# Kernel tuning notes

Measured on AMD Instinct MI355X. Metric: run time of the kernel, lower is better.

## Reference

```python
import jax, jax.numpy as jnp
import numpy as np

NUM_ITERATIONS = 10
ALPHA = 0.1


def setup_inputs() -> dict:
    key = jax.random.key(0)
    k1, k2, k3, k4 = jax.random.split(key, 4)
    N, E, F_IN, H = 100000, 3200000, 512, 64
    x = jax.random.normal(k1, (N, F_IN), dtype=jnp.float32)
    edge_index = jax.random.randint(k2, (2, E), 0, N, dtype=jnp.int32)
    edge_weight = jnp.ones((E,), dtype=jnp.float32)
    # glorot-ish scaled dense weights
    W0 = jax.random.normal(k3, (F_IN, H), dtype=jnp.float32) * (2.0 / (F_IN + H)) ** 0.5
    b0 = jnp.zeros((H,), dtype=jnp.float32)
    W1 = jax.random.normal(k4, (H, H), dtype=jnp.float32) * (2.0 / (H + H)) ** 0.5
    b1 = jnp.zeros((H,), dtype=jnp.float32)
    return {"x": x, "edge_index": edge_index, "edge_weight": edge_weight,
            "W0": W0, "b0": b0, "W1": W1, "b1": b1}


def _gcn_norm_edge(edge_index, edge_weight, num_nodes):
    # renorm: add self-loops with weight 1, then symmetric D^-1/2 A D^-1/2
    row, col = edge_index[0], edge_index[1]
    loop = jnp.arange(num_nodes, dtype=edge_index.dtype)
    row = jnp.concatenate([row, loop])
    col = jnp.concatenate([col, loop])
    w = jnp.concatenate([edge_weight, jnp.ones((num_nodes,), edge_weight.dtype)])
    deg = jax.ops.segment_sum(w, row, num_segments=num_nodes)
    dinv = jnp.where(deg > 0, jax.lax.rsqrt(jnp.where(deg > 0, deg, 1.0)), 0.0)
    w_norm = dinv[row] * w * dinv[col]
    return row, col, w_norm


def reference(x, edge_index, edge_weight, W0, b0, W1, b1):
    N = x.shape[0]
    # MLP: hidden layers relu-activated, last layer unactivated
    h = jax.nn.relu(x @ W0 + b0)
    h = h @ W1 + b1  # [N, H]

    row, col, w_norm = _gcn_norm_edge(edge_index, edge_weight, N)

    def step(z, _):
        # sparse propagation: gather at source, weight, scatter-add at dest
        msg = z[row] * w_norm[:, None]                      # [E+N, H]
        agg = jax.ops.segment_sum(msg, col, num_segments=N)  # [N, H]
        return (1.0 - ALPHA) * agg + ALPHA * h, None

    z, _ = jax.lax.scan(step, h, None, length=NUM_ITERATIONS)
    return z
```

## Files before the change

kernel.cpp:

```cpp
#include <hip/hip_runtime.h>


#define PAGE 16128
#define BPP 64

typedef __attribute__((ext_vector_type(8))) short bf16x8;
typedef __attribute__((ext_vector_type(4))) float f32x4;

__device__ __forceinline__ float bf_lo(unsigned z) { return __uint_as_float(z << 16); }
__device__ __forceinline__ float bf_hi(unsigned z) { return __uint_as_float(z & 0xffff0000u); }
__device__ __forceinline__ unsigned bf_rne(float x) {
    unsigned u = __float_as_uint(x);
    return (u + 0x7fffu + ((u >> 16) & 1u)) >> 16;
}
__device__ __forceinline__ unsigned bf_pack(float x, float y) { return bf_rne(x) | (bf_rne(y) << 16); }

__global__ __launch_bounds__(256) void k_deg(const int* __restrict__ row, const float* __restrict__ ew,
                                             float* __restrict__ slab, int E, int chunk) {
    __shared__ float hf[PAGE];
    int p = blockIdx.x / BPP, b = blockIdx.x - p * BPP;
    int lo = p * PAGE;
    for (int i = threadIdx.x; i < PAGE; i += 256) hf[i] = 0.f;
    __syncthreads();
    int e0 = b * chunk, e1 = min(e0 + chunk, E);
    int evec = e0 + ((e1 - e0) & ~3);
    for (int e = e0 + (int)threadIdx.x * 4; e + 4 <= evec; e += 1024) {
        int4 r4 = *(const int4*)(row + e);
        float4 w4 = *(const float4*)(ew + e);
        unsigned a = (unsigned)(r4.x - lo), bq = (unsigned)(r4.y - lo);
        unsigned c = (unsigned)(r4.z - lo), dq = (unsigned)(r4.w - lo);
        if (a < PAGE) atomicAdd(&hf[a], w4.x);
        if (bq < PAGE) atomicAdd(&hf[bq], w4.y);
        if (c < PAGE) atomicAdd(&hf[c], w4.z);
        if (dq < PAGE) atomicAdd(&hf[dq], w4.w);
    }
    for (int e = evec + (int)threadIdx.x; e < e1; e += 256) {
        unsigned a = (unsigned)(row[e] - lo);
        if (a < PAGE) atomicAdd(&hf[a], ew[e]);
    }
    __syncthreads();
    float* out = slab + (size_t)blockIdx.x * PAGE;
    for (int i = threadIdx.x; i < PAGE; i += 256) out[i] = hf[i];
}

__global__ __launch_bounds__(256) void k_fold_deg(const float* __restrict__ slab, float* __restrict__ dinv, int N) {
    int i = blockIdx.x * 256 + threadIdx.x;
    if (i >= N) return;
    int p = i / PAGE, ld = i - p * PAGE;
    const float* base = slab + (size_t)(p * BPP) * PAGE + ld;
    float d = 1.0f;
#pragma unroll
    for (int b = 0; b < BPP; ++b) d += base[(size_t)b * PAGE];
    dinv[i] = d > 0.f ? rsqrtf(d) : 0.f;
}

__global__ __launch_bounds__(256) void k_cnt(const int* __restrict__ col, unsigned short* __restrict__ slab,
                                             int E, int chunk) {
    __shared__ int hi[PAGE];
    int p = blockIdx.x / BPP, b = blockIdx.x - p * BPP;
    int lo = p * PAGE;
    for (int i = threadIdx.x; i < PAGE; i += 256) hi[i] = 0;
    __syncthreads();
    int e0 = b * chunk, e1 = min(e0 + chunk, E);
    int evec = e0 + ((e1 - e0) & ~3);
    for (int e = e0 + (int)threadIdx.x * 4; e + 4 <= evec; e += 1024) {
        int4 c4 = *(const int4*)(col + e);
        unsigned a = (unsigned)(c4.x - lo), bq = (unsigned)(c4.y - lo);
        unsigned c = (unsigned)(c4.z - lo), dq = (unsigned)(c4.w - lo);
        if (a < PAGE) atomicAdd(&hi[a], 1);
        if (bq < PAGE) atomicAdd(&hi[bq], 1);
        if (c < PAGE) atomicAdd(&hi[c], 1);
        if (dq < PAGE) atomicAdd(&hi[dq], 1);
    }
    for (int e = evec + (int)threadIdx.x; e < e1; e += 256) {
        unsigned a = (unsigned)(col[e] - lo);
        if (a < PAGE) atomicAdd(&hi[a], 1);
    }
    __syncthreads();
    unsigned short* out = slab + (size_t)blockIdx.x * PAGE;
    for (int i = threadIdx.x; i < PAGE; i += 256) out[i] = (unsigned short)hi[i];
}

__global__ __launch_bounds__(256) void k_fold_cnt(unsigned short* __restrict__ slab, int* __restrict__ cnt, int N) {
    int i = blockIdx.x * 256 + threadIdx.x;
    if (i >= N) return;
    int p = i / PAGE, ld = i - p * PAGE;
    unsigned short* base = slab + (size_t)(p * BPP) * PAGE + ld;
    int run = 0;
#pragma unroll
    for (int b = 0; b < BPP; ++b) {
        size_t off = (size_t)b * PAGE;
        int v = base[off];
        base[off] = (unsigned short)run;
        run += v;
    }
    cnt[i] = run;
}

__global__ __launch_bounds__(256) void k_scanA(const int* __restrict__ cnt, int* __restrict__ csum, int N) {
    __shared__ int s[256];
    int t = threadIdx.x, base = blockIdx.x * 1024;
    int p = 0;
#pragma unroll
    for (int j = 0; j < 4; ++j) { int idx = base + t + 256 * j; if (idx < N) p += cnt[idx]; }
    s[t] = p; __syncthreads();
    for (int off = 128; off > 0; off >>= 1) { if (t < off) s[t] += s[t + off]; __syncthreads(); }
    if (t == 0) csum[blockIdx.x] = s[0];
}

__global__ __launch_bounds__(256) void k_scanB(int* __restrict__ csum, int NC) {
    __shared__ int s[256];
    int t = threadIdx.x;
    int v = (t < NC) ? csum[t] : 0;
    s[t] = v; __syncthreads();
    for (int off = 1; off < 256; off <<= 1) {
        int x = (t >= off) ? s[t - off] : 0;
        __syncthreads();
        s[t] += x; __syncthreads();
    }
    if (t < NC) csum[t] = s[t] - v;
}

__global__ __launch_bounds__(256) void k_scanC(const int* __restrict__ cnt, const int* __restrict__ csum,
                                               int* __restrict__ rowp, int N) {
    __shared__ int s[256];
    int t = threadIdx.x, base = blockIdx.x * 1024 + t * 4;
    int c0 = (base + 0 < N) ? cnt[base + 0] : 0;
    int c1 = (base + 1 < N) ? cnt[base + 1] : 0;
    int c2 = (base + 2 < N) ? cnt[base + 2] : 0;
    int c3 = (base + 3 < N) ? cnt[base + 3] : 0;
    int ts = c0 + c1 + c2 + c3;
    s[t] = ts; __syncthreads();
    for (int off = 1; off < 256; off <<= 1) {
        int x = (t >= off) ? s[t - off] : 0;
        __syncthreads();
        s[t] += x; __syncthreads();
    }
    int o = csum[blockIdx.x] + s[t] - ts;
    if (base + 0 < N) rowp[base + 0] = o;
    if (base + 1 < N) rowp[base + 1] = o + c0;
    if (base + 2 < N) rowp[base + 2] = o + c0 + c1;
    if (base + 3 < N) rowp[base + 3] = o + c0 + c1 + c2;
}

__global__ __launch_bounds__(256) void k_scat(const int* __restrict__ row, const int* __restrict__ col,
                                              const float* __restrict__ ew, const float* __restrict__ dinv,
                                              const int* __restrict__ rowp, const unsigned short* __restrict__ slab,
                                              unsigned* __restrict__ srcw, int E, int chunk) {
    __shared__ int cur[PAGE];
    int p = blockIdx.x / BPP, b = blockIdx.x - p * BPP;
    int lo = p * PAGE;
    for (int i = threadIdx.x; i < PAGE; i += 256) cur[i] = 0;
    __syncthreads();
    const unsigned short* soff = slab + (size_t)blockIdx.x * PAGE;
    int e0 = b * chunk, e1 = min(e0 + chunk, E);
    int evec = e0 + ((e1 - e0) & ~3);
    for (int e = e0 + (int)threadIdx.x * 4; e + 4 <= evec; e += 1024) {
        int4 c4 = *(const int4*)(col + e);
        unsigned a = (unsigned)(c4.x - lo), bq = (unsigned)(c4.y - lo);
        unsigned cc = (unsigned)(c4.z - lo), dq = (unsigned)(c4.w - lo);
        if ((a < PAGE) | (bq < PAGE) | (cc < PAGE) | (dq < PAGE)) {
            int4 r4 = *(const int4*)(row + e);
            float4 w4 = *(const float4*)(ew + e);
            if (a < PAGE) {
                int pos = rowp[c4.x] + soff[a] + atomicAdd(&cur[a], 1);
                srcw[pos] = ((unsigned)r4.x << 15) | (bf_rne(dinv[r4.x] * w4.x) & 0x7fffu);
            }
            if (bq < PAGE) {
                int pos = rowp[c4.y] + soff[bq] + atomicAdd(&cur[bq], 1);
                srcw[pos] = ((unsigned)r4.y << 15) | (bf_rne(dinv[r4.y] * w4.y) & 0x7fffu);
            }
            if (cc < PAGE) {
                int pos = rowp[c4.z] + soff[cc] + atomicAdd(&cur[cc], 1);
                srcw[pos] = ((unsigned)r4.z << 15) | (bf_rne(dinv[r4.z] * w4.z) & 0x7fffu);
            }
            if (dq < PAGE) {
                int pos = rowp[c4.w] + soff[dq] + atomicAdd(&cur[dq], 1);
                srcw[pos] = ((unsigned)r4.w << 15) | (bf_rne(dinv[r4.w] * w4.w) & 0x7fffu);
            }
        }
    }
    for (int e = evec + (int)threadIdx.x; e < e1; e += 256) {
        int c = col[e];
        unsigned a = (unsigned)(c - lo);
        if (a < PAGE) {
            int r = row[e];
            int pos = rowp[c] + soff[a] + atomicAdd(&cur[a], 1);
            srcw[pos] = ((unsigned)r << 15) | (bf_rne(dinv[r] * ew[e]) & 0x7fffu);
        }
    }
}

__global__ __launch_bounds__(256) void k_wcvt(const float* __restrict__ W,
                                              unsigned short* __restrict__ Th, unsigned short* __restrict__ Tl,
                                              int K, int total) {
    int i = blockIdx.x * 256 + threadIdx.x;
    if (i >= total) return;
    int k = i >> 6, n = i & 63;
    float v = W[i];
    unsigned hi = bf_rne(v);
    float hv = __uint_as_float(hi << 16);
    unsigned lo = bf_rne(v - hv);
    Th[(size_t)n * K + k] = (unsigned short)hi;
    Tl[(size_t)n * K + k] = (unsigned short)lo;
}

__global__ __launch_bounds__(256) void k_mlp(const float* __restrict__ x,
                                             const unsigned short* __restrict__ w0th, const unsigned short* __restrict__ w0tl,
                                             const unsigned short* __restrict__ w1th, const unsigned short* __restrict__ w1tl,
                                             const float* __restrict__ b0, const float* __restrict__ b1,
                                             unsigned* __restrict__ hb, int N) {
    __shared__ __align__(16) unsigned short h1h[64 * 72];
    __shared__ __align__(16) unsigned short h1l[64 * 72];
    int tid = threadIdx.x;
    int w = tid >> 6, lane = tid & 63;
    int g = lane >> 4, r16 = lane & 15;
    int rbase = blockIdx.x * 64;
    int arow = rbase + w * 16 + r16;
    bool rowok = arow < N;
    const float* xp = x + (size_t)arow * 512 + g * 8;

    f32x4 acc[4];
#pragma unroll
    for (int t = 0; t < 4; ++t) acc[t] = (f32x4){0.f, 0.f, 0.f, 0.f};

    for (int ks = 0; ks < 16; ++ks) {
        int k0 = ks * 32;
        float4 v0 = make_float4(0.f, 0.f, 0.f, 0.f), v1 = v0;
        if (rowok) {
            v0 = *(const float4*)(xp + k0);
            v1 = *(const float4*)(xp + k0 + 4);
        }
        float xv[8] = {v0.x, v0.y, v0.z, v0.w, v1.x, v1.y, v1.z, v1.w};
        bf16x8 xh, xl;
#pragma unroll
        for (int e = 0; e < 8; ++e) {
            float xe = xv[e];
            unsigned hi = bf_rne(xe);
            float hv = __uint_as_float(hi << 16);
            unsigned lo = bf_rne(xe - hv);
            xh[e] = (short)hi;
            xl[e] = (short)lo;
        }
#pragma unroll
        for (int t = 0; t < 4; ++t) {
            size_t wo = (size_t)(t * 16 + r16) * 512 + k0 + g * 8;
            bf16x8 wh = *(const bf16x8*)(w0th + wo);
            bf16x8 wl = *(const bf16x8*)(w0tl + wo);
            acc[t] = __builtin_amdgcn_mfma_f32_16x16x32_bf16(xh, wh, acc[t], 0, 0, 0);
            acc[t] = __builtin_amdgcn_mfma_f32_16x16x32_bf16(xl, wh, acc[t], 0, 0, 0);
            acc[t] = __builtin_amdgcn_mfma_f32_16x16x32_bf16(xh, wl, acc[t], 0, 0, 0);
        }
    }
#pragma unroll
    for (int t = 0; t < 4; ++t) {
        int c = t * 16 + r16;
        float bb = b0[c];
#pragma unroll
        for (int r = 0; r < 4; ++r) {
            float v = fmaxf(acc[t][r] + bb, 0.f);
            unsigned hi = bf_rne(v);
            float hv = __uint_as_float(hi << 16);
            unsigned lo = bf_rne(v - hv);
            int rr = w * 16 + g * 4 + r;
            h1h[rr * 72 + c] = (unsigned short)hi;
            h1l[rr * 72 + c] = (unsigned short)lo;
        }
    }
    __syncthreads();
    f32x4 acc2[4];
#pragma unroll
    for (int t = 0; t < 4; ++t) acc2[t] = (f32x4){0.f, 0.f, 0.f, 0.f};
#pragma unroll
    for (int ks = 0; ks < 2; ++ks) {
        int k0 = ks * 32;
        const unsigned short* ap = h1h + (w * 16 + r16) * 72 + k0 + g * 8;
        bf16x8 ah = *(const bf16x8*)ap;
        bf16x8 al = *(const bf16x8*)(ap + 64 * 72);
        al = *(const bf16x8*)(h1l + (w * 16 + r16) * 72 + k0 + g * 8);
#pragma unroll
        for (int t = 0; t < 4; ++t) {
            size_t wo = (size_t)(t * 16 + r16) * 64 + k0 + g * 8;
            bf16x8 wh = *(const bf16x8*)(w1th + wo);
            bf16x8 wl = *(const bf16x8*)(w1tl + wo);
            acc2[t] = __builtin_amdgcn_mfma_f32_16x16x32_bf16(ah, wh, acc2[t], 0, 0, 0);
            acc2[t] = __builtin_amdgcn_mfma_f32_16x16x32_bf16(al, wh, acc2[t], 0, 0, 0);
            acc2[t] = __builtin_amdgcn_mfma_f32_16x16x32_bf16(ah, wl, acc2[t], 0, 0, 0);
        }
    }
    unsigned short* hb16 = (unsigned short*)hb;
#pragma unroll
    for (int t = 0; t < 4; ++t) {
        int c = t * 16 + r16;
        float bb = b1[c];
#pragma unroll
        for (int r = 0; r < 4; ++r) {
            int grow = rbase + w * 16 + g * 4 + r;
            if (grow < N) {
                float v = acc2[t][r] + bb;
                hb16[(size_t)grow * 64 + c] = (unsigned short)bf_rne(v);
            }
        }
    }
}

__global__ __launch_bounds__(256) void k_prop(const unsigned* __restrict__ srcw,
                                              const int* __restrict__ rowp, const int* __restrict__ cnt,
                                              const float* __restrict__ dinv,
                                              const unsigned* __restrict__ zin, const unsigned* __restrict__ hb,
                                              unsigned* __restrict__ zout_b, float* __restrict__ zout_f, int N) {
    int wid = (blockIdx.x << 2) | (threadIdx.x >> 6);
    int d = __builtin_amdgcn_readfirstlane(wid);
    if (d >= N) return;
    int lane = threadIdx.x & 63;
    int half = lane >> 5, fi = lane & 31;
    int beg = rowp[d], end = beg + cnt[d];
    float ax = 0.f, ay = 0.f;
    for (int e = beg + half; e < end; e += 16) {
        unsigned pk[8];
#pragma unroll
        for (int k = 0; k < 8; ++k) {
            int idx = e + 2 * k;
            pk[k] = srcw[min(idx, end - 1)];
        }
        unsigned z[8];
#pragma unroll
        for (int k = 0; k < 8; ++k) z[k] = zin[(pk[k] >> 15) * 32u + fi];
#pragma unroll
        for (int k = 0; k < 8; ++k) {
            float w = (e + 2 * k < end) ? __uint_as_float((pk[k] & 0x7fffu) << 16) : 0.f;
            ax = fmaf(w, bf_lo(z[k]), ax);
            ay = fmaf(w, bf_hi(z[k]), ay);
        }
    }
    ax += __shfl_xor(ax, 32);
    ay += __shfl_xor(ay, 32);
    if (half == 0) {
        float di = dinv[d];
        unsigned zs = zin[(size_t)d * 32 + fi];
        float s2 = di * di;
        float ox = 0.9f * fmaf(di, ax, s2 * bf_lo(zs));
        float oy = 0.9f * fmaf(di, ay, s2 * bf_hi(zs));
        unsigned hz = hb[(size_t)d * 32 + fi];
        ox = fmaf(0.1f, bf_lo(hz), ox);
        oy = fmaf(0.1f, bf_hi(hz), oy);
        if (zout_f) ((float2*)zout_f)[(size_t)d * 32 + fi] = make_float2(ox, oy);
        else zout_b[(size_t)d * 32 + fi] = bf_pack(ox, oy);
    }
}

extern "C" void kernel_launch(void* const* d_in, const int* in_sizes, int n_in,
                              void* d_out, int out_size, void* d_ws, size_t ws_size,
                              hipStream_t stream) {
    const float* x  = (const float*)d_in[0];
    const int*   ei = (const int*)d_in[1];
    const float* ew = (const float*)d_in[2];
    const float* W0 = (const float*)d_in[3];
    const float* b0 = (const float*)d_in[4];
    const float* W1 = (const float*)d_in[5];
    const float* b1 = (const float*)d_in[6];
    int N = in_sizes[0] / 512;
    int E = in_sizes[2];
    const int* row = ei;
    const int* col = ei + E;

    char* p = (char*)d_ws;
    auto alloc = [&](size_t bytes) -> char* {
        char* r = p;
        p += (bytes + 255) & ~(size_t)255;
        return r;
    };
    int NPg = (N + PAGE - 1) / PAGE;
    size_t zbytes = (size_t)N * 32 * 4;
    size_t slab_bytes = (size_t)NPg * BPP * PAGE * 4;
    unsigned* hb  = (unsigned*)alloc(zbytes);
    float* slabf  = (float*)alloc(slab_bytes);
    unsigned* srcw = (unsigned*)alloc((size_t)E * 4);
    float* dinv  = (float*)alloc((size_t)N * 4);
    int* cnt     = (int*)alloc((size_t)N * 4);
    int* rowp    = (int*)alloc((size_t)N * 4);
    int* csum    = (int*)alloc(512 * 4);
    unsigned short* w0th = (unsigned short*)alloc(64 * 512 * 2);
    unsigned short* w0tl = (unsigned short*)alloc(64 * 512 * 2);
    unsigned short* w1th = (unsigned short*)alloc(64 * 64 * 2);
    unsigned short* w1tl = (unsigned short*)alloc(64 * 64 * 2);
    unsigned short* slabu = (unsigned short*)slabf;
    unsigned* zb0 = (unsigned*)slabf;
    unsigned* zb1 = (unsigned*)((char*)slabf + zbytes);

    int gN = (N + 255) / 256;
    int NC = (N + 1023) / 1024;
    int chunk = (((E + BPP - 1) / BPP) + 3) & ~3;
    int gridPg = NPg * BPP;

    k_wcvt<<<(512 * 64 + 255) / 256, 256, 0, stream>>>(W0, w0th, w0tl, 512, 512 * 64);
    k_wcvt<<<(64 * 64 + 255) / 256, 256, 0, stream>>>(W1, w1th, w1tl, 64, 64 * 64);
    k_deg<<<gridPg, 256, 0, stream>>>(row, ew, slabf, E, chunk);
    k_fold_deg<<<gN, 256, 0, stream>>>(slabf, dinv, N);
    k_cnt<<<gridPg, 256, 0, stream>>>(col, slabu, E, chunk);
    k_fold_cnt<<<gN, 256, 0, stream>>>(slabu, cnt, N);
    k_scanA<<<NC, 256, 0, stream>>>(cnt, csum, N);
    k_scanB<<<1, 256, 0, stream>>>(csum, NC);
    k_scanC<<<NC, 256, 0, stream>>>(cnt, csum, rowp, N);
    k_scat<<<gridPg, 256, 0, stream>>>(row, col, ew, dinv, rowp, slabu, srcw, E, chunk);
    k_mlp<<<(N + 63) / 64, 256, 0, stream>>>(x, w0th, w0tl, w1th, w1tl, b0, b1, hb, N);

    unsigned* zbufs[2] = { zb0, zb1 };
    const unsigned* zi = hb;
    int gP = (N + 3) / 4;
    for (int it = 0; it < 10; ++it) {
        if (it < 9) {
            unsigned* zo = zbufs[it & 1];
            k_prop<<<gP, 256, 0, stream>>>(srcw, rowp, cnt, dinv, zi, hb, zo, nullptr, N);
            zi = zo;
        } else {
            k_prop<<<gP, 256, 0, stream>>>(srcw, rowp, cnt, dinv, zi, hb, nullptr, (float*)d_out, N);
        }
    }
}
```

Baseline: 1.216 ms.

## Stage x tiles through LDS with coalesced loads in MLP kernel; merge weight conversion launches

The first MLP layer now loads 128-column chunks of x with row-contiguous float4 loads by all threads, splits each value into truncated hi and rounded lo bf16 parts, stores both in padded shared memory, and has MFMA operands read from LDS. This replaces strided per-lane global loads that each covered only 32 columns per row. The hidden-layer split also switches from round-to-nearest hi to truncation, the LDS buffers are reused for the second layer, and the two weight-conversion launches are merged into one. The extra barriers and larger LDS footprint may limit occupancy, and the launch-bounds hint asks for four blocks per SM.

Measured after the change: 1.235 ms. No clear change (+1.6%).

```diff
diff --git a/kernel.cpp b/kernel.cpp
--- a/kernel.cpp
+++ b/kernel.cpp
@@ -3,6 +3,7 @@
 
 #define PAGE 16128
 #define BPP 64
+#define XST 136
 
 typedef __attribute__((ext_vector_type(8))) short bf16x8;
 typedef __attribute__((ext_vector_type(4))) float f32x4;
@@ -191,66 +192,94 @@
     }
 }
 
-__global__ __launch_bounds__(256) void k_wcvt(const float* __restrict__ W,
-                                              unsigned short* __restrict__ Th, unsigned short* __restrict__ Tl,
-                                              int K, int total) {
+__global__ __launch_bounds__(256) void k_wcvt(const float* __restrict__ W0, const float* __restrict__ W1,
+                                              unsigned short* __restrict__ Th0, unsigned short* __restrict__ Tl0,
+                                              unsigned short* __restrict__ Th1, unsigned short* __restrict__ Tl1) {
     int i = blockIdx.x * 256 + threadIdx.x;
-    if (i >= total) return;
-    int k = i >> 6, n = i & 63;
-    float v = W[i];
+    float v;
+    unsigned short *th, *tl;
+    size_t o;
+    if (i < 512 * 64) {
+        int k = i >> 6, n = i & 63;
+        v = W0[i];
+        th = Th0; tl = Tl0; o = (size_t)n * 512 + k;
+    } else {
+        int j = i - 512 * 64;
+        if (j >= 64 * 64) return;
+        int k = j >> 6, n = j & 63;
+        v = W1[j];
+        th = Th1; tl = Tl1; o = (size_t)n * 64 + k;
+    }
     unsigned hi = bf_rne(v);
     float hv = __uint_as_float(hi << 16);
     unsigned lo = bf_rne(v - hv);
-    Th[(size_t)n * K + k] = (unsigned short)hi;
-    Tl[(size_t)n * K + k] = (unsigned short)lo;
-}
-
-__global__ __launch_bounds__(256) void k_mlp(const float* __restrict__ x,
-                                             const unsigned short* __restrict__ w0th, const unsigned short* __restrict__ w0tl,
-                                             const unsigned short* __restrict__ w1th, const unsigned short* __restrict__ w1tl,
-                                             const float* __restrict__ b0, const float* __restrict__ b1,
-                                             unsigned* __restrict__ hb, int N) {
-    __shared__ __align__(16) unsigned short h1h[64 * 72];
-    __shared__ __align__(16) unsigned short h1l[64 * 72];
+    th[o] = (unsigned short)hi;
+    tl[o] = (unsigned short)lo;
+}
+
+__global__ __launch_bounds__(256, 4) void k_mlp(const float* __restrict__ x,
+                                                const unsigned short* __restrict__ w0th, const unsigned short* __restrict__ w0tl,
+                                                const unsigned short* __restrict__ w1th, const unsigned short* __restrict__ w1tl,
+                                                const float* __restrict__ b0, const float* __restrict__ b1,
+                                                unsigned* __restrict__ hb, int N) {
+    __shared__ __align__(16) unsigned short xh[64 * XST];
+    __shared__ __align__(16) unsigned short xl[64 * XST];
     int tid = threadIdx.x;
     int w = tid >> 6, lane = tid & 63;
     int g = lane >> 4, r16 = lane & 15;
     int rbase = blockIdx.x * 64;
-    int arow = rbase + w * 16 + r16;
-    bool rowok = arow < N;
-    const float* xp = x + (size_t)arow * 512 + g * 8;
+
+    int srow = tid >> 2, sseg = tid & 3;
+    bool sok = rbase + srow < N;
+    const float* xrow = x + (size_t)(rbase + srow) * 512 + sseg * 4;
 
     f32x4 acc[4];
 #pragma unroll
     for (int t = 0; t < 4; ++t) acc[t] = (f32x4){0.f, 0.f, 0.f, 0.f};
 
-    for (int ks = 0; ks < 16; ++ks) {
-        int k0 = ks * 32;
-        float4 v0 = make_float4(0.f, 0.f, 0.f, 0.f), v1 = v0;
-        if (rowok) {
-            v0 = *(const float4*)(xp + k0);
-            v1 = *(const float4*)(xp + k0 + 4);
-        }
-        float xv[8] = {v0.x, v0.y, v0.z, v0.w, v1.x, v1.y, v1.z, v1.w};
-        bf16x8 xh, xl;
-#pragma unroll
-        for (int e = 0; e < 8; ++e) {
-            float xe = xv[e];
-            unsigned hi = bf_rne(xe);
-            float hv = __uint_as_float(hi << 16);
-            unsigned lo = bf_rne(xe - hv);
-            xh[e] = (short)hi;
-            xl[e] = (short)lo;
-        }
-#pragma unroll
-        for (int t = 0; t < 4; ++t) {
-            size_t wo = (size_t)(t * 16 + r16) * 512 + k0 + g * 8;
-            bf16x8 wh = *(const bf16x8*)(w0th + wo);
-            bf16x8 wl = *(const bf16x8*)(w0tl + wo);
-            acc[t] = __builtin_amdgcn_mfma_f32_16x16x32_bf16(xh, wh, acc[t], 0, 0, 0);
-            acc[t] = __builtin_amdgcn_mfma_f32_16x16x32_bf16(xl, wh, acc[t], 0, 0, 0);
-            acc[t] = __builtin_amdgcn_mfma_f32_16x16x32_bf16(xh, wl, acc[t], 0, 0, 0);
-        }
+    for (int kc = 0; kc < 4; ++kc) {
+        int k0c = kc * 128;
+        float4 v[8];
+#pragma unroll
+        for (int i = 0; i < 8; ++i)
+            v[i] = sok ? *(const float4*)(xrow + k0c + i * 16) : make_float4(0.f, 0.f, 0.f, 0.f);
+#pragma unroll
+        for (int i = 0; i < 8; ++i) {
+            float e0 = v[i].x, e1 = v[i].y, e2 = v[i].z, e3 = v[i].w;
+            unsigned u0 = __float_as_uint(e0), u1 = __float_as_uint(e1);
+            unsigned u2 = __float_as_uint(e2), u3 = __float_as_uint(e3);
+            unsigned short h0 = (unsigned short)(u0 >> 16), h1q = (unsigned short)(u1 >> 16);
+            unsigned short h2 = (unsigned short)(u2 >> 16), h3 = (unsigned short)(u3 >> 16);
+            float l0 = e0 - __uint_as_float(u0 & 0xffff0000u);
+            float l1 = e1 - __uint_as_float(u1 & 0xffff0000u);
+            float l2 = e2 - __uint_as_float(u2 & 0xffff0000u);
+            float l3 = e3 - __uint_as_float(u3 & 0xffff0000u);
+            int o = srow * XST + sseg * 4 + i * 16;
+            ushort4 hv4 = make_ushort4(h0, h1q, h2, h3);
+            ushort4 lv4 = make_ushort4((unsigned short)bf_rne(l0), (unsigned short)bf_rne(l1),
+                                       (unsigned short)bf_rne(l2), (unsigned short)bf_rne(l3));
+            *(ushort4*)(xh + o) = hv4;
+            *(ushort4*)(xl + o) = lv4;
+        }
+        __syncthreads();
+#pragma unroll
+        for (int ks = 0; ks < 4; ++ks) {
+            int kk = ks * 32 + g * 8;
+            const unsigned short* ab = xh + (w * 16 + r16) * XST + kk;
+            bf16x8 ah = *(const bf16x8*)ab;
+            bf16x8 al = *(const bf16x8*)(xl + (w * 16 + r16) * XST + kk);
+            int kg = k0c + kk;
+#pragma unroll
+            for (int t = 0; t < 4; ++t) {
+                size_t wo = (size_t)(t * 16 + r16) * 512 + kg;
+                bf16x8 wh = *(const bf16x8*)(w0th + wo);
+                bf16x8 wl = *(const bf16x8*)(w0tl + wo);
+                acc[t] = __builtin_amdgcn_mfma_f32_16x16x32_bf16(ah, wh, acc[t], 0, 0, 0);
+                acc[t] = __builtin_amdgcn_mfma_f32_16x16x32_bf16(al, wh, acc[t], 0, 0, 0);
+                acc[t] = __builtin_amdgcn_mfma_f32_16x16x32_bf16(ah, wl, acc[t], 0, 0, 0);
+            }
+        }
+        __syncthreads();
     }
 #pragma unroll
     for (int t = 0; t < 4; ++t) {
@@ -258,13 +287,13 @@
         float bb = b0[c];
 #pragma unroll
         for (int r = 0; r < 4; ++r) {
-            float v = fmaxf(acc[t][r] + bb, 0.f);
-            unsigned hi = bf_rne(v);
-            float hv = __uint_as_float(hi << 16);
-            unsigned lo = bf_rne(v - hv);
+            float vv = fmaxf(acc[t][r] + bb, 0.f);
+            unsigned u = __float_as_uint(vv);
+            unsigned short hi = (unsigned short)(u >> 16);
+            float lo = vv - __uint_as_float(u & 0xffff0000u);
             int rr = w * 16 + g * 4 + r;
-            h1h[rr * 72 + c] = (unsigned short)hi;
-            h1l[rr * 72 + c] = (unsigned short)lo;
+            xh[rr * 72 + c] = hi;
+            xl[rr * 72 + c] = (unsigned short)bf_rne(lo);
         }
     }
     __syncthreads();
@@ -273,14 +302,12 @@
     for (int t = 0; t < 4; ++t) acc2[t] = (f32x4){0.f, 0.f, 0.f, 0.f};
 #pragma unroll
     for (int ks = 0; ks < 2; ++ks) {
-        int k0 = ks * 32;
-        const unsigned short* ap = h1h + (w * 16 + r16) * 72 + k0 + g * 8;
-        bf16x8 ah = *(const bf16x8*)ap;
-        bf16x8 al = *(const bf16x8*)(ap + 64 * 72);
-        al = *(const bf16x8*)(h1l + (w * 16 + r16) * 72 + k0 + g * 8);
+        int k0 = ks * 32 + g * 8;
+        bf16x8 ah = *(const bf16x8*)(xh + (w * 16 + r16) * 72 + k0);
+        bf16x8 al = *(const bf16x8*)(xl + (w * 16 + r16) * 72 + k0);
 #pragma unroll
         for (int t = 0; t < 4; ++t) {
-            size_t wo = (size_t)(t * 16 + r16) * 64 + k0 + g * 8;
+            size_t wo = (size_t)(t * 16 + r16) * 64 + k0;
             bf16x8 wh = *(const bf16x8*)(w1th + wo);
             bf16x8 wl = *(const bf16x8*)(w1tl + wo);
             acc2[t] = __builtin_amdgcn_mfma_f32_16x16x32_bf16(ah, wh, acc2[t], 0, 0, 0);
@@ -297,8 +324,8 @@
         for (int r = 0; r < 4; ++r) {
             int grow = rbase + w * 16 + g * 4 + r;
             if (grow < N) {
-                float v = acc2[t][r] + bb;
-                hb16[(size_t)grow * 64 + c] = (unsigned short)bf_rne(v);
+                float vv = acc2[t][r] + bb;
+                hb16[(size_t)grow * 64 + c] = (unsigned short)bf_rne(vv);
             }
         }
     }
@@ -393,8 +420,7 @@
     int chunk = (((E + BPP - 1) / BPP) + 3) & ~3;
     int gridPg = NPg * BPP;
 
-    k_wcvt<<<(512 * 64 + 255) / 256, 256, 0, stream>>>(W0, w0th, w0tl, 512, 512 * 64);
-    k_wcvt<<<(64 * 64 + 255) / 256, 256, 0, stream>>>(W1, w1th, w1tl, 64, 64 * 64);
+    k_wcvt<<<(512 * 64 + 64 * 64 + 255) / 256, 256, 0, stream>>>(W0, W1, w0th, w0tl, w1th, w1tl);
     k_deg<<<gridPg, 256, 0, stream>>>(row, ew, slabf, E, chunk);
     k_fold_deg<<<gN, 256, 0, stream>>>(slabf, dinv, N);
     k_cnt<<<gridPg, 256, 0, stream>>>(col, slabu, E, chunk);
```
